# Kernel tuning notes

Measured on AMD Instinct MI355X. Metric: run time of the kernel, lower is better.

Reference implementation:

```python
import jax, jax.numpy as jnp
import numpy as np

BT, C, H, W = 16, 64, 128, 128
K, S = 16, 8            # ksize, stride2
MID = C // 2            # BasicBlock mid channels
INTER = C // 1          # r = 1 -> inter_channels = channels
NH = (H - K) // S + 1
NW = (W - K) // S + 1
L = NH * NW             # 225 patches


def _lrelu(x):
    return jnp.where(x > 0, x, 0.2 * x)


def _conv(x, w):
    return jax.lax.conv_general_dilated(
        x, w, window_strides=(1, 1), padding='VALID',
        dimension_numbers=('NCHW', 'OIHW', 'NCHW'))


def setup_inputs() -> dict:
    key = jax.random.key(0)
    ks = jax.random.split(key, 7)
    fea = jax.random.normal(ks[0], (BT, C, H, W), jnp.float32)
    spa_graph = jax.random.normal(ks[1], (BT, L, L), jnp.float32) * 0.05
    spe_graph = jax.random.normal(ks[2], (BT, C, C), jnp.float32) * 0.05
    W1 = jax.random.normal(ks[3], (MID, C, 3, 3), jnp.float32) * 0.05
    W2 = jax.random.normal(ks[4], (C, MID, 1, 1), jnp.float32) * 0.05
    Wl = jax.random.normal(ks[5], (INTER, C, 1, 1), jnp.float32) * 0.05
    bl = jnp.zeros((INTER,), jnp.float32)
    return {'fea': fea, 'spa_graph': spa_graph, 'spe_graph': spe_graph,
            'W1': W1, 'W2': W2, 'Wl': Wl, 'bl': bl}


def reference(fea, spa_graph, spe_graph, W1, W2, Wl, bl):
    bt, c, h, w = fea.shape
    # BasicBlock: reflect-pad conv3x3 -> lrelu -> conv1x1 -> lrelu
    xp = jnp.pad(fea, ((0, 0), (0, 0), (1, 1), (1, 1)), mode='reflect')
    f = _lrelu(_conv(_lrelu(_conv(xp, W1)), W2))            # [bt,c,h,w]

    # unfold (torch.nn.Unfold order: (C, kh, kw) feature-major, row-major patches)
    patches = jax.lax.conv_general_dilated_patches(f, (K, K), (S, S), 'VALID')
    cols = patches.reshape(bt, c * K * K, L)                 # [bt,F,L]

    # per-sample spatial-graph matmul: graph[p,q] @ patches[q,F]
    out_spa = jnp.einsum('bpq,bfq->bfp', spa_graph, cols)    # [bt,F,L]

    # fold: overlap-add patches back to [bt,c,h,w]
    rows = jnp.arange(NH) * S + jnp.arange(K)[:, None]       # [K,NH]
    colsi = jnp.arange(NW) * S + jnp.arange(K)[:, None]      # [K,NW]
    lin = (rows[:, None, :, None] * w + colsi[None, :, None, :]).reshape(-1)
    vals = out_spa.reshape(bt, c, K * K * L)
    x = jnp.zeros((bt, c, h * w), fea.dtype).at[:, :, lin].add(vals)
    x = x.reshape(bt, c, h, w)

    # per-sample spectral-graph matmul
    residual = jnp.einsum('bcd,bdn->bcn', spe_graph,
                          f.reshape(bt, c, h * w)).reshape(bt, c, h, w)

    xa = 0.5 * (x + residual)
    xl = _lrelu(_conv(xa, Wl) + bl[None, :, None, None])
    wei = jax.nn.sigmoid(xl)
    return x * wei + residual * (1.0 - wei) + f
```

## Files before the change

kernel.cpp:

```cpp
#include <hip/hip_runtime.h>
#include <hip/hip_bf16.h>
#include <hip/hip_runtime_api.h>

#define BT 16
#define CCH 64
#define H 128
#define W 128
#define STR 8
#define NH 15
#define NW 15
#define L 225
#define HW (H * W)

#define UPITCH 264
#define RP 72
#define CP 72
#define MP 40

typedef __attribute__((ext_vector_type(8))) short short8;
typedef __attribute__((ext_vector_type(4))) float f32x4;
typedef __attribute__((ext_vector_type(4))) unsigned short ushort4_t;

__device__ __forceinline__ float lrelu(float v) { return v > 0.f ? v : 0.2f * v; }
__device__ __forceinline__ unsigned short f2bf(float v) {
  __hip_bfloat16 h = __float2bfloat16(v);
  unsigned short u;
  __builtin_memcpy(&u, &h, 2);
  return u;
}
__device__ __forceinline__ float bf2f(unsigned short u) {
  unsigned int x = ((unsigned int)u) << 16;
  float f;
  __builtin_memcpy(&f, &x, 4);
  return f;
}

__global__ __launch_bounds__(256) void prep_all_k(
    const float* __restrict__ fea, const float* __restrict__ spa,
    const float* __restrict__ W1, const float* __restrict__ W2,
    const float* __restrict__ spe, const float* __restrict__ Wl,
    __hip_bfloat16* __restrict__ ft, __hip_bfloat16* __restrict__ T,
    __hip_bfloat16* __restrict__ W1r, __hip_bfloat16* __restrict__ W2r,
    __hip_bfloat16* __restrict__ spe_r, __hip_bfloat16* __restrict__ wl_r) {
  const int bid = blockIdx.x;
  const int tid = threadIdx.x;

  if (bid < 1024) {
    const int lb = (bid % 8) * 128 + bid / 8;
    const int b = lb >> 6;
    const int p0 = (lb & 63) * 256;
#pragma unroll 1
    for (int it = 0; it < 8; ++it) {
      const int u = it * 256 + tid;
      const int px = u >> 3, g = u & 7;
      const int p = p0 + px;
      short8 v;
#pragma unroll
      for (int j = 0; j < 8; ++j)
        v[j] = (short)f2bf(fea[((size_t)b * CCH + g * 8 + j) * HW + p]);
      *(short8*)&ft[((size_t)b * HW + p) * CCH + g * 8] = v;
    }
    return;
  }

  if (bid < 5120) {
    const int bp = bid - 1024;
    const int b = bp >> 8, pi = bp & 255;
    const int k = tid;
    const int yi = pi >> 4, xi = pi & 15;
    const int ky = k >> 4, kx = k & 15;
    const float* sb = spa + (size_t)b * L * L;
    float acc = 0.f;
#pragma unroll
    for (int vy = 0; vy < 2; ++vy)
#pragma unroll
      for (int vx = 0; vx < 2; ++vx) {
        const int py = yi - vy, px = xi - vx;
        const int qy = ky - vy, qx = kx - vx;
        if (py >= 0 && py < NH && px >= 0 && px < NW && qy >= 0 && qy < NH &&
            qx >= 0 && qx < NW)
          acc += sb[(py * NW + px) * L + qy * NW + qx];
      }
    T[(size_t)bp * 256 + k] = __float2bfloat16(acc);
    return;
  }

  const int idx = (bid - 5120) * 256 + tid;
  if (idx < 18432) {
    const int kk = idx >> 10, mc = (idx >> 5) & 31, ck = idx & 31;
    const int pos = kk >> 1, s = kk & 1;
    W1r[idx] = __float2bfloat16(W1[(mc * 64 + s * 32 + ck) * 9 + pos]);
    return;
  }
  int i = idx - 18432;
  if (i < 2048) { W2r[i] = __float2bfloat16(W2[i]); return; }
  i -= 2048;
  if (i < BT * CCH * CCH) { spe_r[i] = __float2bfloat16(spe[i]); return; }
  i -= BT * CCH * CCH;
  if (i < CCH * CCH) { wl_r[i] = __float2bfloat16(Wl[i]); return; }
}

__global__ __launch_bounds__(512) void bblock_mfma_k(
    const __hip_bfloat16* __restrict__ ft, const __hip_bfloat16* __restrict__ W1r,
    const __hip_bfloat16* __restrict__ W2r, __hip_bfloat16* __restrict__ fnh) {
  __shared__ __align__(16) short sbuf[324 * CP];
  short* st = sbuf;
  short* mids = sbuf;
  unsigned short* fst = (unsigned short*)sbuf;

  const int lb = ((int)blockIdx.x % 8) * 128 + (int)blockIdx.x / 8;
  const int b = lb >> 6;
  const int tile = lb & 63;
  const int ty0 = (tile >> 3) * 16, tx0 = (tile & 7) * 16;
  const int tid = threadIdx.x;

  for (int i = tid; i < 2592; i += 512) {
    const int px = i >> 3, g = i & 7;
    const int iy = px / 18, ix = px - iy * 18;
    int gy = ty0 + iy - 1;
    gy = gy < 0 ? -gy : (gy > 127 ? 254 - gy : gy);
    int gx = tx0 + ix - 1;
    gx = gx < 0 ? -gx : (gx > 127 ? 254 - gx : gx);
    *(short8*)&st[px * CP + g * 8] =
        *(const short8*)&ft[((size_t)b * HW + gy * W + gx) * CCH + g * 8];
  }
  __syncthreads();

  const int w = tid >> 6, lane = tid & 63, lm = lane & 15, lk = lane >> 4;
  const short* w1 = (const short*)W1r;
  const short* w2 = (const short*)W2r;

  f32x4 acc[2][2];
#pragma unroll
  for (int mt = 0; mt < 2; ++mt)
#pragma unroll
    for (int t = 0; t < 2; ++t) acc[mt][t] = (f32x4){0.f, 0.f, 0.f, 0.f};

#pragma unroll
  for (int pos = 0; pos < 9; ++pos) {
    const int dy = pos / 3, dx = pos - dy * 3;
#pragma unroll
    for (int s = 0; s < 2; ++s) {
      short8 a0 = *(const short8*)&w1[((pos * 2 + s) * 32 + lm) * 32 + lk * 8];
      short8 a1 = *(const short8*)&w1[((pos * 2 + s) * 32 + 16 + lm) * 32 + lk * 8];
#pragma unroll
      for (int t = 0; t < 2; ++t) {
        const int p = (w * 2 + t + dy) * 18 + lm + dx;
        short8 bb = *(const short8*)&st[p * CP + s * 32 + lk * 8];
        acc[0][t] = __builtin_amdgcn_mfma_f32_16x16x32_bf16(a0, bb, acc[0][t], 0, 0, 0);
        acc[1][t] = __builtin_amdgcn_mfma_f32_16x16x32_bf16(a1, bb, acc[1][t], 0, 0, 0);
      }
    }
  }

  __syncthreads();

#pragma unroll
  for (int t = 0; t < 2; ++t) {
    const int n = (w * 2 + t) * 16 + lm;
#pragma unroll
    for (int mt = 0; mt < 2; ++mt) {
      ushort4_t pk;
#pragma unroll
      for (int r = 0; r < 4; ++r) pk[r] = f2bf(lrelu(acc[mt][t][r]));
      *(ushort4_t*)&mids[n * MP + mt * 16 + lk * 4] = pk;
    }
  }
  __syncthreads();

  f32x4 acc2[4][2];
#pragma unroll
  for (int m2 = 0; m2 < 4; ++m2)
#pragma unroll
    for (int t = 0; t < 2; ++t) acc2[m2][t] = (f32x4){0.f, 0.f, 0.f, 0.f};

  short8 b2[2];
#pragma unroll
  for (int t = 0; t < 2; ++t)
    b2[t] = *(const short8*)&mids[((w * 2 + t) * 16 + lm) * MP + lk * 8];
#pragma unroll
  for (int m2 = 0; m2 < 4; ++m2) {
    short8 a2 = *(const short8*)&w2[(m2 * 16 + lm) * 32 + lk * 8];
#pragma unroll
    for (int t = 0; t < 2; ++t)
      acc2[m2][t] = __builtin_amdgcn_mfma_f32_16x16x32_bf16(a2, b2[t], acc2[m2][t], 0, 0, 0);
  }

  __syncthreads();

#pragma unroll
  for (int m2 = 0; m2 < 4; ++m2)
#pragma unroll
    for (int t = 0; t < 2; ++t) {
      ushort4_t pk;
#pragma unroll
      for (int r = 0; r < 4; ++r) pk[r] = f2bf(lrelu(acc2[m2][t][r]));
      *(ushort4_t*)&fst[((w * 2 + t) * 16 + lm) * RP + m2 * 16 + lk * 4] = pk;
    }
  __syncthreads();

  unsigned short* fo = (unsigned short*)fnh;
  for (int i = tid; i < 2048; i += 512) {
    const int lp = i >> 3, g = i & 7;
    const int y = ty0 + (lp >> 4), x = tx0 + (lp & 15);
    *(short8*)&fo[((size_t)b * HW + y * W + x) * CCH + g * 8] =
        *(const short8*)&fst[lp * RP + g * 8];
  }
}

__global__ __launch_bounds__(512) void spa_mfma_k(
    const __hip_bfloat16* __restrict__ fnh, const __hip_bfloat16* __restrict__ T,
    __hip_bfloat16* __restrict__ xnh) {
  __shared__ __align__(16) short us[256 * RP];

  const int lb = ((int)blockIdx.x % 8) * 128 + (int)blockIdx.x / 8;
  const int b = lb >> 6, ky0 = (lb >> 3) & 7, kx0 = lb & 7;
  const int tid = threadIdx.x;

  const unsigned short* fb = (const unsigned short*)fnh + (size_t)b * HW * CCH;

  for (int i = tid; i < 2048; i += 512) {
    const int pos = i >> 3, g = i & 7;
    const int gy = pos >> 4, gx = pos & 15;
    const int blk = pos >> 3;
    short8 v = *(const short8*)&fb[((ky0 + 8 * gy) * W + kx0 + 8 * gx) * CCH + g * 8];
#pragma unroll
    for (int e = 0; e < 8; ++e) {
      const int c = g * 8 + e;
      const int sblk = (blk & ~7) | ((blk ^ (c >> 3)) & 7);
      us[c * UPITCH + sblk * 8 + (pos & 7)] = v[e];
    }
  }
  __syncthreads();

  const int w = tid >> 6, lane = tid & 63;
  const int lm = lane & 15, lk = lane >> 4;
  const int mtg = w >> 2, ntg = w & 3;

  const short* tb = (const short*)T + (size_t)b * 256 * 256;

  f32x4 acc[2][4];
#pragma unroll
  for (int mt = 0; mt < 2; ++mt)
#pragma unroll
    for (int n = 0; n < 4; ++n) acc[mt][n] = (f32x4){0.f, 0.f, 0.f, 0.f};

  const int c0 = (mtg * 2) * 16 + lm, c1 = (mtg * 2 + 1) * 16 + lm;

#pragma unroll
  for (int k8 = 0; k8 < 8; ++k8) {
    const int kb = k8 * 4 + lk;
    const int sb0 = (kb & ~7) | ((kb ^ (c0 >> 3)) & 7);
    const int sb1 = (kb & ~7) | ((kb ^ (c1 >> 3)) & 7);
    short8 a0 = *(const short8*)&us[c0 * UPITCH + sb0 * 8];
    short8 a1 = *(const short8*)&us[c1 * UPITCH + sb1 * 8];
    short8 bb[4];
#pragma unroll
    for (int n = 0; n < 4; ++n)
      bb[n] = *(const short8*)&tb[((ntg * 4 + n) * 16 + lm) * 256 + k8 * 32 + lk * 8];
#pragma unroll
    for (int n = 0; n < 4; ++n) {
      acc[0][n] = __builtin_amdgcn_mfma_f32_16x16x32_bf16(a0, bb[n], acc[0][n], 0, 0, 0);
      acc[1][n] = __builtin_amdgcn_mfma_f32_16x16x32_bf16(a1, bb[n], acc[1][n], 0, 0, 0);
    }
  }

  __syncthreads();

  unsigned short* xst = (unsigned short*)us;
#pragma unroll
  for (int mt = 0; mt < 2; ++mt)
#pragma unroll
    for (int n = 0; n < 4; ++n) {
      ushort4_t pk;
#pragma unroll
      for (int r = 0; r < 4; ++r) pk[r] = f2bf(acc[mt][n][r]);
      *(ushort4_t*)&xst[((ntg * 4 + n) * 16 + lm) * RP + (mtg * 2 + mt) * 16 + lk * 4] = pk;
    }
  __syncthreads();

  unsigned short* xo = (unsigned short*)xnh + (size_t)b * HW * CCH;
  for (int i = tid; i < 2048; i += 512) {
    const int pi = i >> 3, g = i & 7;
    const int row = (pi >> 4) * 8 + ky0;
    const int col = (pi & 15) * 8 + kx0;
    *(short8*)&xo[((size_t)row * W + col) * CCH + g * 8] =
        *(const short8*)&xst[pi * RP + g * 8];
  }
}

__global__ __launch_bounds__(256) void final_mfma_k(
    const __hip_bfloat16* __restrict__ fnh, const __hip_bfloat16* __restrict__ xnh,
    const __hip_bfloat16* __restrict__ spe_r, const __hip_bfloat16* __restrict__ wl_r,
    const float* __restrict__ bl, float* __restrict__ xo) {
  __shared__ __align__(16) short fl[128 * CP];
  __shared__ __align__(16) short xal[128 * CP];
  const int lb = ((int)blockIdx.x % 8) * 256 + (int)blockIdx.x / 8;
  const int b = lb >> 7;
  const int px0 = (lb & 127) * 128;
  const int tid = threadIdx.x;

  for (int i = tid; i < 128 * 8; i += 256) {
    const int px = i >> 3, g = i & 7;
    *(short8*)&fl[px * CP + g * 8] =
        *(const short8*)&fnh[((size_t)b * HW + px0 + px) * CCH + g * 8];
  }
  __syncthreads();

  const int w = tid >> 6, lane = tid & 63, lm = lane & 15, lk = lane >> 4;
  const int c0 = w * 16 + lk * 4;

  const short* sa = (const short*)spe_r + ((size_t)b * CCH + w * 16 + lm) * CCH;
  const short8 a1_0 = *(const short8*)&sa[lk * 8];
  const short8 a1_1 = *(const short8*)&sa[32 + lk * 8];

  const unsigned short* xb = (const unsigned short*)xnh + (size_t)b * HW * CCH;

  f32x4 res[8];
  f32x4 xar[8];
#pragma unroll
  for (int nt = 0; nt < 8; ++nt) {
    const int prow = (nt * 16 + lm) * CP;
    short8 b0 = *(const short8*)&fl[prow + lk * 8];
    short8 b1 = *(const short8*)&fl[prow + 32 + lk * 8];
    f32x4 r = (f32x4){0.f, 0.f, 0.f, 0.f};
    r = __builtin_amdgcn_mfma_f32_16x16x32_bf16(a1_0, b0, r, 0, 0, 0);
    r = __builtin_amdgcn_mfma_f32_16x16x32_bf16(a1_1, b1, r, 0, 0, 0);
    res[nt] = r;
    ushort4_t xq = *(const ushort4_t*)&xb[(size_t)(px0 + nt * 16 + lm) * CCH + c0];
    ushort4_t pk;
    f32x4 xa;
#pragma unroll
    for (int j = 0; j < 4; ++j) {
      xa[j] = 0.5f * (bf2f(xq[j]) + r[j]);
      pk[j] = f2bf(xa[j]);
    }
    xar[nt] = xa;
    *(ushort4_t*)&xal[(nt * 16 + lm) * CP + c0] = pk;
  }
  __syncthreads();

  const short* wa = (const short*)wl_r + (w * 16 + lm) * CCH;
  const short8 a2_0 = *(const short8*)&wa[lk * 8];
  const short8 a2_1 = *(const short8*)&wa[32 + lk * 8];
  float blv[4];
#pragma unroll
  for (int j = 0; j < 4; ++j) blv[j] = bl[c0 + j];

#pragma unroll
  for (int nt = 0; nt < 8; ++nt) {
    const int prow = (nt * 16 + lm) * CP;
    short8 b0 = *(const short8*)&xal[prow + lk * 8];
    short8 b1 = *(const short8*)&xal[prow + 32 + lk * 8];
    f32x4 t = (f32x4){0.f, 0.f, 0.f, 0.f};
    t = __builtin_amdgcn_mfma_f32_16x16x32_bf16(a2_0, b0, t, 0, 0, 0);
    t = __builtin_amdgcn_mfma_f32_16x16x32_bf16(a2_1, b1, t, 0, 0, 0);
    ushort4_t fpk = *(const ushort4_t*)&fl[prow + c0];
#pragma unroll
    for (int j = 0; j < 4; ++j) {
      const float xl = lrelu(t[j] + blv[j]);
      const float wei = 1.f / (1.f + __expf(-xl));
      const float o = 2.f * xar[nt][j] * wei + res[nt][j] * (1.f - 2.f * wei) +
                      bf2f(fpk[j]);
      xo[((size_t)b * CCH + c0 + j) * HW + px0 + nt * 16 + lm] = o;
    }
  }
}

extern "C" void kernel_launch(void* const* d_in, const int* in_sizes, int n_in,
                              void* d_out, int out_size, void* d_ws,
                              size_t ws_size, hipStream_t stream) {
  const float* fea = (const float*)d_in[0];
  const float* spa = (const float*)d_in[1];
  const float* spe = (const float*)d_in[2];
  const float* W1  = (const float*)d_in[3];
  const float* W2  = (const float*)d_in[4];
  const float* Wl  = (const float*)d_in[5];
  const float* bl  = (const float*)d_in[6];
  float* out = (float*)d_out;

  const size_t FT_BYTES  = (size_t)BT * HW * CCH * 2;
  const size_t FNH_BYTES = (size_t)BT * HW * CCH * 2;
  const size_t T_BYTES   = (size_t)BT * 256 * 256 * 2;
  char* wsb = (char*)d_ws;
  __hip_bfloat16* ft  = (__hip_bfloat16*)wsb;
  __hip_bfloat16* xnh = (__hip_bfloat16*)wsb;
  __hip_bfloat16* fnh = (__hip_bfloat16*)(wsb + FT_BYTES);
  __hip_bfloat16* T   = (__hip_bfloat16*)(wsb + FT_BYTES + FNH_BYTES);
  char* wtb = wsb + FT_BYTES + FNH_BYTES + T_BYTES;
  __hip_bfloat16* W1r   = (__hip_bfloat16*)wtb;
  __hip_bfloat16* W2r   = (__hip_bfloat16*)(wtb + 36864);
  __hip_bfloat16* spe_r = (__hip_bfloat16*)(wtb + 36864 + 4096);
  __hip_bfloat16* wl_r  = (__hip_bfloat16*)(wtb + 36864 + 4096 + 131072);

  prep_all_k<<<dim3(5472), 256, 0, stream>>>(fea, spa, W1, W2, spe, Wl,
                                             ft, T, W1r, W2r, spe_r, wl_r);
  bblock_mfma_k<<<dim3(1024), 512, 0, stream>>>(ft, W1r, W2r, fnh);
  spa_mfma_k<<<dim3(BT * 64), 512, 0, stream>>>(fnh, T, xnh);
  final_mfma_k<<<dim3(2048), 256, 0, stream>>>(fnh, xnh, spe_r, wl_r, bl, out);
}
```

Measured before the change: 126.4 us.

## Fuse fp32-to-bf16 NHWC transpose into conv tile load; stage x tile in LDS

The separate prep pass that converted fea to a bf16 channel-last buffer is removed. The BasicBlock kernel now reads fp32 NCHW rows directly with float4 loads, converts to bf16 and scatters into its LDS halo tile, and fixes the reflect-padded edge columns with an extra pass. This drops a full write and read of the intermediate tensor. Separately, the final kernel now loads the x tile into LDS alongside f and reuses that buffer for the xa values, replacing per-thread strided global loads. The cost is scalar transposing LDS stores with likely bank conflicts and extra barriers for edge tiles.

```diff
diff --git a/kernel.cpp b/kernel.cpp
--- a/kernel.cpp
+++ b/kernel.cpp
@@ -36,35 +36,16 @@
 }
 
 __global__ __launch_bounds__(256) void prep_all_k(
-    const float* __restrict__ fea, const float* __restrict__ spa,
-    const float* __restrict__ W1, const float* __restrict__ W2,
-    const float* __restrict__ spe, const float* __restrict__ Wl,
-    __hip_bfloat16* __restrict__ ft, __hip_bfloat16* __restrict__ T,
+    const float* __restrict__ spa, const float* __restrict__ W1,
+    const float* __restrict__ W2, const float* __restrict__ spe,
+    const float* __restrict__ Wl, __hip_bfloat16* __restrict__ T,
     __hip_bfloat16* __restrict__ W1r, __hip_bfloat16* __restrict__ W2r,
     __hip_bfloat16* __restrict__ spe_r, __hip_bfloat16* __restrict__ wl_r) {
   const int bid = blockIdx.x;
   const int tid = threadIdx.x;
 
-  if (bid < 1024) {
-    const int lb = (bid % 8) * 128 + bid / 8;
-    const int b = lb >> 6;
-    const int p0 = (lb & 63) * 256;
-#pragma unroll 1
-    for (int it = 0; it < 8; ++it) {
-      const int u = it * 256 + tid;
-      const int px = u >> 3, g = u & 7;
-      const int p = p0 + px;
-      short8 v;
-#pragma unroll
-      for (int j = 0; j < 8; ++j)
-        v[j] = (short)f2bf(fea[((size_t)b * CCH + g * 8 + j) * HW + p]);
-      *(short8*)&ft[((size_t)b * HW + p) * CCH + g * 8] = v;
-    }
-    return;
-  }
-
-  if (bid < 5120) {
-    const int bp = bid - 1024;
+  if (bid < 4096) {
+    const int bp = bid;
     const int b = bp >> 8, pi = bp & 255;
     const int k = tid;
     const int yi = pi >> 4, xi = pi & 15;
@@ -85,7 +66,7 @@
     return;
   }
 
-  const int idx = (bid - 5120) * 256 + tid;
+  const int idx = (bid - 4096) * 256 + tid;
   if (idx < 18432) {
     const int kk = idx >> 10, mc = (idx >> 5) & 31, ck = idx & 31;
     const int pos = kk >> 1, s = kk & 1;
@@ -101,7 +82,7 @@
 }
 
 __global__ __launch_bounds__(512) void bblock_mfma_k(
-    const __hip_bfloat16* __restrict__ ft, const __hip_bfloat16* __restrict__ W1r,
+    const float* __restrict__ fea, const __hip_bfloat16* __restrict__ W1r,
     const __hip_bfloat16* __restrict__ W2r, __hip_bfloat16* __restrict__ fnh) {
   __shared__ __align__(16) short sbuf[324 * CP];
   short* st = sbuf;
@@ -114,15 +95,37 @@
   const int ty0 = (tile >> 3) * 16, tx0 = (tile & 7) * 16;
   const int tid = threadIdx.x;
 
-  for (int i = tid; i < 2592; i += 512) {
-    const int px = i >> 3, g = i & 7;
-    const int iy = px / 18, ix = px - iy * 18;
+  const int txm1 = tx0 - 1;
+  const int qbase = (tx0 == 0) ? 0 : tx0 - 4;
+  const int nq = ((tx0 == 0) | (tx0 == 112)) ? 5 : 6;
+  const int rowlen = 18 * nq;
+  for (int i = tid; i < 64 * rowlen; i += 512) {
+    const int c = i / rowlen;
+    const int r = i - c * rowlen;
+    const int iy = r / nq, q = r - iy * nq;
     int gy = ty0 + iy - 1;
     gy = gy < 0 ? -gy : (gy > 127 ? 254 - gy : gy);
-    int gx = tx0 + ix - 1;
-    gx = gx < 0 ? -gx : (gx > 127 ? 254 - gx : gx);
-    *(short8*)&st[px * CP + g * 8] =
-        *(const short8*)&ft[((size_t)b * HW + gy * W + gx) * CCH + g * 8];
+    const f32x4 v = *(const f32x4*)&fea[((size_t)(b * CCH + c) * H + gy) * W +
+                                        qbase + q * 4];
+#pragma unroll
+    for (int j = 0; j < 4; ++j) {
+      const int ix = qbase + q * 4 + j - txm1;
+      if (ix >= 0 && ix < 18)
+        st[(iy * 18 + ix) * CP + c] = (short)f2bf(v[j]);
+    }
+  }
+  if (tx0 == 0) {
+    __syncthreads();
+    for (int i = tid; i < 64 * 18; i += 512) {
+      const int c = i / 18, iy = i - (i / 18) * 18;
+      st[(iy * 18 + 0) * CP + c] = st[(iy * 18 + 2) * CP + c];
+    }
+  } else if (tx0 == 112) {
+    __syncthreads();
+    for (int i = tid; i < 64 * 18; i += 512) {
+      const int c = i / 18, iy = i - (i / 18) * 18;
+      st[(iy * 18 + 17) * CP + c] = st[(iy * 18 + 15) * CP + c];
+    }
   }
   __syncthreads();
 
@@ -294,16 +297,19 @@
     const __hip_bfloat16* __restrict__ spe_r, const __hip_bfloat16* __restrict__ wl_r,
     const float* __restrict__ bl, float* __restrict__ xo) {
   __shared__ __align__(16) short fl[128 * CP];
-  __shared__ __align__(16) short xal[128 * CP];
+  __shared__ __align__(16) short xbuf[128 * CP];
   const int lb = ((int)blockIdx.x % 8) * 256 + (int)blockIdx.x / 8;
   const int b = lb >> 7;
   const int px0 = (lb & 127) * 128;
   const int tid = threadIdx.x;
 
+  const unsigned short* xg = (const unsigned short*)xnh + (size_t)b * HW * CCH;
   for (int i = tid; i < 128 * 8; i += 256) {
     const int px = i >> 3, g = i & 7;
     *(short8*)&fl[px * CP + g * 8] =
         *(const short8*)&fnh[((size_t)b * HW + px0 + px) * CCH + g * 8];
+    *(short8*)&xbuf[px * CP + g * 8] =
+        *(const short8*)&xg[(size_t)(px0 + px) * CCH + g * 8];
   }
   __syncthreads();
 
@@ -314,7 +320,7 @@
   const short8 a1_0 = *(const short8*)&sa[lk * 8];
   const short8 a1_1 = *(const short8*)&sa[32 + lk * 8];
 
-  const unsigned short* xb = (const unsigned short*)xnh + (size_t)b * HW * CCH;
+  unsigned short* xbu = (unsigned short*)xbuf;
 
   f32x4 res[8];
   f32x4 xar[8];
@@ -327,7 +333,7 @@
     r = __builtin_amdgcn_mfma_f32_16x16x32_bf16(a1_0, b0, r, 0, 0, 0);
     r = __builtin_amdgcn_mfma_f32_16x16x32_bf16(a1_1, b1, r, 0, 0, 0);
     res[nt] = r;
-    ushort4_t xq = *(const ushort4_t*)&xb[(size_t)(px0 + nt * 16 + lm) * CCH + c0];
+    ushort4_t xq = *(const ushort4_t*)&xbu[prow + c0];
     ushort4_t pk;
     f32x4 xa;
 #pragma unroll
@@ -336,7 +342,7 @@
       pk[j] = f2bf(xa[j]);
     }
     xar[nt] = xa;
-    *(ushort4_t*)&xal[(nt * 16 + lm) * CP + c0] = pk;
+    *(ushort4_t*)&xbu[prow + c0] = pk;
   }
   __syncthreads();
 
@@ -350,8 +356,8 @@
 #pragma unroll
   for (int nt = 0; nt < 8; ++nt) {
     const int prow = (nt * 16 + lm) * CP;
-    short8 b0 = *(const short8*)&xal[prow + lk * 8];
-    short8 b1 = *(const short8*)&xal[prow + 32 + lk * 8];
+    short8 b0 = *(const short8*)&xbuf[prow + lk * 8];
+    short8 b1 = *(const short8*)&xbuf[prow + 32 + lk * 8];
     f32x4 t = (f32x4){0.f, 0.f, 0.f, 0.f};
     t = __builtin_amdgcn_mfma_f32_16x16x32_bf16(a2_0, b0, t, 0, 0, 0);
     t = __builtin_amdgcn_mfma_f32_16x16x32_bf16(a2_1, b1, t, 0, 0, 0);
@@ -379,23 +385,22 @@
   const float* bl  = (const float*)d_in[6];
   float* out = (float*)d_out;
 
-  const size_t FT_BYTES  = (size_t)BT * HW * CCH * 2;
+  const size_t XNH_BYTES = (size_t)BT * HW * CCH * 2;
   const size_t FNH_BYTES = (size_t)BT * HW * CCH * 2;
   const size_t T_BYTES   = (size_t)BT * 256 * 256 * 2;
   char* wsb = (char*)d_ws;
-  __hip_bfloat16* ft  = (__hip_bfloat16*)wsb;
   __hip_bfloat16* xnh = (__hip_bfloat16*)wsb;
-  __hip_bfloat16* fnh = (__hip_bfloat16*)(wsb + FT_BYTES);
-  __hip_bfloat16* T   = (__hip_bfloat16*)(wsb + FT_BYTES + FNH_BYTES);
-  char* wtb = wsb + FT_BYTES + FNH_BYTES + T_BYTES;
+  __hip_bfloat16* fnh = (__hip_bfloat16*)(wsb + XNH_BYTES);
+  __hip_bfloat16* T   = (__hip_bfloat16*)(wsb + XNH_BYTES + FNH_BYTES);
+  char* wtb = wsb + XNH_BYTES + FNH_BYTES + T_BYTES;
   __hip_bfloat16* W1r   = (__hip_bfloat16*)wtb;
   __hip_bfloat16* W2r   = (__hip_bfloat16*)(wtb + 36864);
   __hip_bfloat16* spe_r = (__hip_bfloat16*)(wtb + 36864 + 4096);
   __hip_bfloat16* wl_r  = (__hip_bfloat16*)(wtb + 36864 + 4096 + 131072);
 
-  prep_all_k<<<dim3(5472), 256, 0, stream>>>(fea, spa, W1, W2, spe, Wl,
-                                             ft, T, W1r, W2r, spe_r, wl_r);
-  bblock_mfma_k<<<dim3(1024), 512, 0, stream>>>(ft, W1r, W2r, fnh);
+  prep_all_k<<<dim3(4448), 256, 0, stream>>>(spa, W1, W2, spe, Wl,
+                                             T, W1r, W2r, spe_r, wl_r);
+  bblock_mfma_k<<<dim3(1024), 512, 0, stream>>>(fea, W1r, W2r, fnh);
   spa_mfma_k<<<dim3(BT * 64), 512, 0, stream>>>(fnh, T, xnh);
   final_mfma_k<<<dim3(2048), 256, 0, stream>>>(fnh, xnh, spe_r, wl_r, bl, out);
 }
```

Result: faster. 120.2 us (-4.9%).
